# Kernel tuning notes

Measured on AMD Instinct MI355X. Metric: run time of the kernel, lower is better.

The kernel has to match this reference:

```python
import jax, jax.numpy as jnp
import numpy as np

EMBED_DIM = 1024
NUM_HEADS = 16
HEAD_DIM = EMBED_DIM // NUM_HEADS


def setup_inputs() -> dict:
    key = jax.random.key(0)
    k1, k2, k3, k4 = jax.random.split(key, 4)
    B, T, C = 4, 2048, EMBED_DIM
    scale = 1.0 / np.sqrt(C)
    x = jax.random.normal(k1, (B, T, C), dtype=jnp.float32)
    # nn.Linear(C, 3C, bias=False): weight [3C, C]
    w_qkv = jax.random.normal(k2, (3 * C, C), dtype=jnp.float32) * scale
    # nn.Linear(C, C) with bias
    w_out = jax.random.normal(k3, (C, C), dtype=jnp.float32) * scale
    b_out = jax.random.normal(k4, (C,), dtype=jnp.float32) * 0.01
    return {"x": x, "w_qkv": w_qkv, "w_out": w_out, "b_out": b_out}


def reference(x, w_qkv, w_out, b_out):
    B, T, C = x.shape
    H, D = NUM_HEADS, HEAD_DIM
    qkv = x @ w_qkv.T                      # [B,T,3C]
    q, k, v = jnp.split(qkv, 3, axis=-1)
    # [B,T,C] -> [B,H,T,D]
    q = q.reshape(B, T, H, D).transpose(0, 2, 1, 3)
    k = k.reshape(B, T, H, D).transpose(0, 2, 1, 3)
    v = v.reshape(B, T, H, D).transpose(0, 2, 1, 3)
    scores = jnp.einsum("bhqd,bhkd->bhqk", q, k) / jnp.sqrt(jnp.float32(D))
    causal = jnp.tril(jnp.ones((T, T), dtype=bool))
    scores = jnp.where(causal, scores, -jnp.inf)
    attn = jax.nn.softmax(scores, axis=-1)  # dropout is identity in eval mode
    out = jnp.einsum("bhqk,bhkd->bhqd", attn, v)
    out = out.transpose(0, 2, 1, 3).reshape(B, T, C)
    return out @ w_out.T + b_out
```

## Files before the change

kernel.cpp:

```cpp
#include <hip/hip_runtime.h>
#include <hip/hip_bf16.h>

typedef __bf16 bf16_t;
typedef __bf16 bf16x4 __attribute__((ext_vector_type(4)));
typedef __bf16 bf16x8 __attribute__((ext_vector_type(8)));
typedef float f32x4 __attribute__((ext_vector_type(4)));

#define MFMA16(a, b, c) __builtin_amdgcn_mfma_f32_16x16x32_bf16(a, b, c, 0, 0, 0)

__device__ __forceinline__ void gld16(const bf16_t* g, bf16_t* l) {
  __builtin_amdgcn_global_load_lds(
      (const __attribute__((address_space(1))) unsigned int*)(const void*)g,
      (__attribute__((address_space(3))) unsigned int*)(void*)l, 16, 0, 0);
}

__global__ __launch_bounds__(256) void cvt_f32_bf16(
    const float* __restrict__ src, bf16_t* __restrict__ dst, long long n) {
  long long i = ((long long)blockIdx.x * 256 + threadIdx.x) * 8;
  const long long stride = (long long)gridDim.x * 256 * 8;
  for (; i < n; i += stride) {
    f32x4 a = *(const f32x4*)(src + i);
    f32x4 b = *(const f32x4*)(src + i + 4);
    bf16x8 r;
#pragma unroll
    for (int e = 0; e < 4; ++e) {
      r[e] = (bf16_t)a[e];
      r[4 + e] = (bf16_t)b[e];
    }
    *(bf16x8*)(dst + i) = r;
  }
}

template <bool WF32, typename TC, bool BIAS>
__global__ __launch_bounds__(256, 2) void gemm_async(
    const bf16_t* __restrict__ A, int lda, const void* __restrict__ Wv,
    const float* __restrict__ bias, TC* __restrict__ C, int ldc,
    int M, int N, int K) {
  constexpr int BST = WF32 ? 40 : 32;
  __shared__ bf16_t As[128 * 32];
  __shared__ bf16_t Bs[128 * BST];

  const int tid = threadIdx.x;
  const int i = tid & 63;
  const int w = tid >> 6;
  const int l16 = tid & 15;
  const int quad = (tid >> 4) & 3;
  const int wm = w & 1;
  const int wn = w >> 1;
  const int m0 = blockIdx.y * 128;
  const int n0 = blockIdx.x * 128;

  const bf16_t* ag = A + (size_t)(m0 + w * 32 + (i >> 2)) * lda + (i & 3) * 8;
  bf16_t* as0 = &As[(w * 32) * 32];
  bf16_t* as1 = &As[(w * 32 + 16) * 32];

  const bf16_t* bg = nullptr;
  bf16_t *bs0 = nullptr, *bs1 = nullptr;
  const float* wfg = nullptr;
  bf16_t* bsw = nullptr;
  if (!WF32) {
    bg = (const bf16_t*)Wv + (size_t)(n0 + w * 32 + (i >> 2)) * K + (i & 3) * 8;
    bs0 = &Bs[(w * 32) * 32];
    bs1 = &Bs[(w * 32 + 16) * 32];
  } else {
    const int srow = tid >> 1;
    const int scol = (tid & 1) * 16;
    wfg = (const float*)Wv + (size_t)(n0 + srow) * K + scol;
    bsw = &Bs[srow * BST + scol];
  }

  f32x4 acc[4][4] = {};

  for (int k0 = 0; k0 < K; k0 += 32) {
    __syncthreads();
    gld16(ag + k0, as0);
    gld16(ag + 16 * lda + k0, as1);
    if (!WF32) {
      gld16(bg + k0, bs0);
      gld16(bg + 16 * K + k0, bs1);
    } else {
      f32x4 a = *(const f32x4*)(wfg + k0);
      f32x4 b = *(const f32x4*)(wfg + k0 + 4);
      f32x4 c2 = *(const f32x4*)(wfg + k0 + 8);
      f32x4 d = *(const f32x4*)(wfg + k0 + 12);
      bf16x8 r0, r1;
#pragma unroll
      for (int e = 0; e < 4; ++e) {
        r0[e] = (bf16_t)a[e];
        r0[4 + e] = (bf16_t)b[e];
        r1[e] = (bf16_t)c2[e];
        r1[4 + e] = (bf16_t)d[e];
      }
      *(bf16x8*)(bsw) = r0;
      *(bf16x8*)(bsw + 8) = r1;
    }
    __syncthreads();

    bf16x8 af[4], bfr[4];
#pragma unroll
    for (int t = 0; t < 4; ++t) {
      af[t] = *(const bf16x8*)&As[(wm * 64 + t * 16 + l16) * 32 + quad * 8];
      bfr[t] = *(const bf16x8*)&Bs[(wn * 64 + t * 16 + l16) * BST + quad * 8];
    }
#pragma unroll
    for (int mi = 0; mi < 4; ++mi)
#pragma unroll
      for (int ni = 0; ni < 4; ++ni)
        acc[mi][ni] = MFMA16(af[mi], bfr[ni], acc[mi][ni]);
  }

#pragma unroll
  for (int ni = 0; ni < 4; ++ni) {
    const int col = n0 + wn * 64 + ni * 16 + l16;
    const float bv = BIAS ? bias[col] : 0.0f;
#pragma unroll
    for (int mi = 0; mi < 4; ++mi) {
      const int row = m0 + wm * 64 + mi * 16 + quad * 4;
#pragma unroll
      for (int r = 0; r < 4; ++r)
        C[(size_t)(row + r) * ldc + col] = (TC)(acc[mi][ni][r] + bv);
    }
  }
}

__global__ __launch_bounds__(512, 4) void attn_mfma(bf16_t* __restrict__ qkv) {
  constexpr int T = 2048, C3 = 3072, C = 1024;
  __shared__ bf16_t Ks[64 * 72];
  __shared__ bf16_t Vt[64 * 72];
  __shared__ bf16_t Ps[8 * 16 * 72];

  const int tid = threadIdx.x;
  const int wave = tid >> 6;
  const int lane = tid & 63;
  const int l16 = tid & 15;
  const int quad = (tid >> 4) & 3;
  const int p = blockIdx.x;
  const int b = blockIdx.y >> 4;
  const int h = blockIdx.y & 15;
  bf16_t* base = qkv + (size_t)b * T * C3;

  const float QSCALE = 0.125f * 1.44269504088896340736f;

  const int kst = tid >> 2;
  const int ksd = (tid & 3) * 16;
  const int vtok = lane;
  const int vdg = (wave - 4) * 16;

  bf16_t* pw = &Ps[wave * 16 * 72];

  bf16x8 st0, st1;

  for (int s = 0; s < 2; ++s) {
    const int qt = (s == 0) ? p : 15 - p;
    const int Q0 = qt * 128;
    const int qlo = Q0 + wave * 16;
    const int jmax = Q0 + 64;

    bf16x8 qf[2];
    {
      const bf16_t* qp = base + (size_t)(qlo + l16) * C3 + h * 64 + quad * 8;
      bf16x8 a = *(const bf16x8*)qp;
      bf16x8 c = *(const bf16x8*)(qp + 32);
#pragma unroll
      for (int e = 0; e < 8; ++e) {
        a[e] = (bf16_t)((float)a[e] * QSCALE);
        c[e] = (bf16_t)((float)c[e] * QSCALE);
      }
      qf[0] = a;
      qf[1] = c;
    }

    f32x4 Of[4] = {};
    float mrow = -1e30f;
    float lrow = 0.f;

    if (wave < 4) {
      const bf16_t* kp = base + (size_t)kst * C3 + C + h * 64 + ksd;
      st0 = *(const bf16x8*)kp;
      st1 = *(const bf16x8*)(kp + 8);
    } else {
      const bf16_t* vp = base + (size_t)vtok * C3 + 2 * C + h * 64 + vdg;
      st0 = *(const bf16x8*)vp;
      st1 = *(const bf16x8*)(vp + 8);
    }

    for (int j0 = 0; j0 <= jmax; j0 += 64) {
      __syncthreads();
      if (wave < 4) {
        *(bf16x8*)&Ks[kst * 72 + ksd] = st0;
        *(bf16x8*)&Ks[kst * 72 + ksd + 8] = st1;
      } else {
#pragma unroll
        for (int e = 0; e < 8; ++e) {
          Vt[(vdg + e) * 72 + vtok] = st0[e];
          Vt[(vdg + 8 + e) * 72 + vtok] = st1[e];
        }
      }
      if (j0 + 64 <= jmax) {
        const int jn = j0 + 64;
        if (wave < 4) {
          const bf16_t* kp = base + (size_t)(jn + kst) * C3 + C + h * 64 + ksd;
          st0 = *(const bf16x8*)kp;
          st1 = *(const bf16x8*)(kp + 8);
        } else {
          const bf16_t* vp =
              base + (size_t)(jn + vtok) * C3 + 2 * C + h * 64 + vdg;
          st0 = *(const bf16x8*)vp;
          st1 = *(const bf16x8*)(vp + 8);
        }
      }
      __syncthreads();

      if (qlo + 15 < j0) continue;

      float Sv[4][4];
      const int qrow = qlo + l16;
      __builtin_amdgcn_s_setprio(1);
#pragma unroll
      for (int nt = 0; nt < 4; ++nt) {
        f32x4 sacc = {};
#pragma unroll
        for (int s2 = 0; s2 < 2; ++s2) {
          bf16x8 kf =
              *(const bf16x8*)&Ks[(nt * 16 + l16) * 72 + s2 * 32 + quad * 8];
          sacc = MFMA16(kf, qf[s2], sacc);
        }
#pragma unroll
        for (int r = 0; r < 4; ++r) Sv[nt][r] = sacc[r];
      }
      __builtin_amdgcn_s_setprio(0);

      if (j0 + 64 > qlo) {
#pragma unroll
        for (int nt = 0; nt < 4; ++nt) {
          const int keyb = j0 + nt * 16 + quad * 4;
#pragma unroll
          for (int r = 0; r < 4; ++r)
            if (keyb + r > qrow) Sv[nt][r] = -1e30f;
        }
      }

      float vm[4];
#pragma unroll
      for (int nt = 0; nt < 4; ++nt)
        vm[nt] = fmaxf(fmaxf(Sv[nt][0], Sv[nt][1]),
                       fmaxf(Sv[nt][2], Sv[nt][3]));
      float v = fmaxf(fmaxf(vm[0], vm[1]), fmaxf(vm[2], vm[3]));
      v = fmaxf(v, __shfl_xor(v, 16));
      v = fmaxf(v, __shfl_xor(v, 32));

      if (__any(v > mrow)) {
        const float mnew = fmaxf(mrow, v);
        const float alpha = __builtin_amdgcn_exp2f(mrow - mnew);
        mrow = mnew;
        lrow *= alpha;
        float ar[4];
#pragma unroll
        for (int r = 0; r < 4; ++r) ar[r] = __shfl(alpha, quad * 4 + r, 16);
#pragma unroll
        for (int dt = 0; dt < 4; ++dt)
#pragma unroll
          for (int r = 0; r < 4; ++r) Of[dt][r] *= ar[r];
      }

      float rsn[4];
#pragma unroll
      for (int nt = 0; nt < 4; ++nt) {
        bf16x4 pk;
        float r0 = __builtin_amdgcn_exp2f(Sv[nt][0] - mrow);
        float r1 = __builtin_amdgcn_exp2f(Sv[nt][1] - mrow);
        float r2 = __builtin_amdgcn_exp2f(Sv[nt][2] - mrow);
        float r3 = __builtin_amdgcn_exp2f(Sv[nt][3] - mrow);
        pk[0] = (bf16_t)r0;
        pk[1] = (bf16_t)r1;
        pk[2] = (bf16_t)r2;
        pk[3] = (bf16_t)r3;
        rsn[nt] = (r0 + r1) + (r2 + r3);
        *(bf16x4*)&pw[l16 * 72 + nt * 16 + quad * 4] = pk;
      }
      float rs = (rsn[0] + rsn[1]) + (rsn[2] + rsn[3]);
      rs += __shfl_xor(rs, 16);
      rs += __shfl_xor(rs, 32);
      lrow += rs;

      bf16x8 pf0 = *(const bf16x8*)&pw[l16 * 72 + quad * 8];
      bf16x8 pf1 = *(const bf16x8*)&pw[l16 * 72 + 32 + quad * 8];
      __builtin_amdgcn_s_setprio(1);
#pragma unroll
      for (int dt = 0; dt < 4; ++dt) {
        bf16x8 vf0 = *(const bf16x8*)&Vt[(dt * 16 + l16) * 72 + quad * 8];
        bf16x8 vf1 = *(const bf16x8*)&Vt[(dt * 16 + l16) * 72 + 32 + quad * 8];
        Of[dt] = MFMA16(pf0, vf0, Of[dt]);
        Of[dt] = MFMA16(pf1, vf1, Of[dt]);
      }
      __builtin_amdgcn_s_setprio(0);
    }

    float lr[4];
#pragma unroll
    for (int r = 0; r < 4; ++r) lr[r] = __shfl(lrow, quad * 4 + r, 16);
    const int t = Q0 + wave * 16 + quad * 4;
#pragma unroll
    for (int r = 0; r < 4; ++r) {
      const float inv = 1.0f / lr[r];
      bf16_t* op = base + (size_t)(t + r) * C3 + h * 64 + l16;
#pragma unroll
      for (int dt = 0; dt < 4; ++dt)
        op[dt * 16] = (bf16_t)(Of[dt][r] * inv);
    }
  }
}

extern "C" void kernel_launch(void* const* d_in, const int* in_sizes, int n_in,
                              void* d_out, int out_size, void* d_ws,
                              size_t ws_size, hipStream_t stream) {
  constexpr int B = 4, T = 2048, C = 1024;
  constexpr int M = B * T;

  const float* x = (const float*)d_in[0];
  const float* w_qkv = (const float*)d_in[1];
  const float* w_out = (const float*)d_in[2];
  const float* b_out = (const float*)d_in[3];
  for (int i = 0; i < n_in; ++i) {
    const long long s = in_sizes[i];
    if (s == (long long)M * C) x = (const float*)d_in[i];
    else if (s == (long long)3 * C * C) w_qkv = (const float*)d_in[i];
    else if (s == (long long)C * C) w_out = (const float*)d_in[i];
    else if (s == C) b_out = (const float*)d_in[i];
  }

  bf16_t* xb = (bf16_t*)d_out;
  bf16_t* wqb = xb + (size_t)M * C;
  bf16_t* qkv = (bf16_t*)d_ws;
  bf16_t* wob = qkv + (size_t)M * 3 * C;
  const bool ws_ok =
      ws_size >= (size_t)M * 3 * C * 2 + (size_t)C * C * 2;

  cvt_f32_bf16<<<1024, 256, 0, stream>>>(x, xb, (long long)M * C);
  cvt_f32_bf16<<<512, 256, 0, stream>>>(w_qkv, wqb, 3LL * C * C);
  if (ws_ok)
    cvt_f32_bf16<<<256, 256, 0, stream>>>(w_out, wob, (long long)C * C);

  gemm_async<false, bf16_t, false>
      <<<dim3(3 * C / 128, M / 128), 256, 0, stream>>>(
          xb, C, wqb, nullptr, qkv, 3 * C, M, 3 * C, C);

  attn_mfma<<<dim3(8, B * 16), 512, 0, stream>>>(qkv);

  if (ws_ok)
    gemm_async<false, float, true><<<dim3(C / 128, M / 128), 256, 0, stream>>>(
        qkv, 3 * C, wob, b_out, (float*)d_out, C, M, C, C);
  else
    gemm_async<true, float, true><<<dim3(C / 128, M / 128), 256, 0, stream>>>(
        qkv, 3 * C, w_out, b_out, (float*)d_out, C, M, C, C);
}
```

Baseline: 265.1 us.

## Double-buffer GEMM LDS tiles, prefetch next K slice, and swizzle workgroup order

Converts the GEMM main loop to a two-stage LDS pipeline: the next K tile is fetched with async global-to-LDS loads, or held in registers for the f32 weight path, while MFMAs run on the current tile. This removes one barrier per iteration and hides load latency. It also remaps workgroup IDs in groups of eight, likely to spread neighbouring tiles across XCDs, and raises wave priority around the MFMA block. The cost is doubled LDS, which may cut occupancy, and extra registers for the prefetched f32 values.

```diff
diff --git a/kernel.cpp b/kernel.cpp
--- a/kernel.cpp
+++ b/kernel.cpp
@@ -37,8 +37,8 @@
     const float* __restrict__ bias, TC* __restrict__ C, int ldc,
     int M, int N, int K) {
   constexpr int BST = WF32 ? 40 : 32;
-  __shared__ bf16_t As[128 * 32];
-  __shared__ bf16_t Bs[128 * BST];
+  __shared__ bf16_t As[2][128 * 32];
+  __shared__ bf16_t Bs[2][128 * BST];
 
   const int tid = threadIdx.x;
   const int i = tid & 63;
@@ -47,66 +47,110 @@
   const int quad = (tid >> 4) & 3;
   const int wm = w & 1;
   const int wn = w >> 1;
-  const int m0 = blockIdx.y * 128;
-  const int n0 = blockIdx.x * 128;
+
+  const int nwg = gridDim.x * gridDim.y;
+  int wg = blockIdx.y * gridDim.x + blockIdx.x;
+  if ((nwg & 7) == 0) wg = (wg & 7) * (nwg >> 3) + (wg >> 3);
+  const int m0 = (wg / gridDim.x) * 128;
+  const int n0 = (wg % gridDim.x) * 128;
 
   const bf16_t* ag = A + (size_t)(m0 + w * 32 + (i >> 2)) * lda + (i & 3) * 8;
-  bf16_t* as0 = &As[(w * 32) * 32];
-  bf16_t* as1 = &As[(w * 32 + 16) * 32];
+  bf16_t* as0[2] = {&As[0][(w * 32) * 32], &As[1][(w * 32) * 32]};
+  bf16_t* as1[2] = {&As[0][(w * 32 + 16) * 32], &As[1][(w * 32 + 16) * 32]};
 
   const bf16_t* bg = nullptr;
-  bf16_t *bs0 = nullptr, *bs1 = nullptr;
+  bf16_t *bs0[2] = {nullptr, nullptr}, *bs1[2] = {nullptr, nullptr};
   const float* wfg = nullptr;
-  bf16_t* bsw = nullptr;
+  bf16_t* bsw[2] = {nullptr, nullptr};
   if (!WF32) {
     bg = (const bf16_t*)Wv + (size_t)(n0 + w * 32 + (i >> 2)) * K + (i & 3) * 8;
-    bs0 = &Bs[(w * 32) * 32];
-    bs1 = &Bs[(w * 32 + 16) * 32];
+    bs0[0] = &Bs[0][(w * 32) * 32];
+    bs0[1] = &Bs[1][(w * 32) * 32];
+    bs1[0] = &Bs[0][(w * 32 + 16) * 32];
+    bs1[1] = &Bs[1][(w * 32 + 16) * 32];
   } else {
     const int srow = tid >> 1;
     const int scol = (tid & 1) * 16;
     wfg = (const float*)Wv + (size_t)(n0 + srow) * K + scol;
-    bsw = &Bs[srow * BST + scol];
+    bsw[0] = &Bs[0][srow * BST + scol];
+    bsw[1] = &Bs[1][srow * BST + scol];
   }
 
   f32x4 acc[4][4] = {};
 
+  gld16(ag, as0[0]);
+  gld16(ag + 16 * lda, as1[0]);
+  if (!WF32) {
+    gld16(bg, bs0[0]);
+    gld16(bg + 16 * K, bs1[0]);
+  } else {
+    f32x4 a = *(const f32x4*)(wfg);
+    f32x4 b = *(const f32x4*)(wfg + 4);
+    f32x4 c2 = *(const f32x4*)(wfg + 8);
+    f32x4 d = *(const f32x4*)(wfg + 12);
+    bf16x8 r0, r1;
+#pragma unroll
+    for (int e = 0; e < 4; ++e) {
+      r0[e] = (bf16_t)a[e];
+      r0[4 + e] = (bf16_t)b[e];
+      r1[e] = (bf16_t)c2[e];
+      r1[4 + e] = (bf16_t)d[e];
+    }
+    *(bf16x8*)(bsw[0]) = r0;
+    *(bf16x8*)(bsw[0] + 8) = r1;
+  }
+  __syncthreads();
+
+  int cur = 0;
   for (int k0 = 0; k0 < K; k0 += 32) {
-    __syncthreads();
-    gld16(ag + k0, as0);
-    gld16(ag + 16 * lda + k0, as1);
-    if (!WF32) {
-      gld16(bg + k0, bs0);
-      gld16(bg + 16 * K + k0, bs1);
-    } else {
-      f32x4 a = *(const f32x4*)(wfg + k0);
-      f32x4 b = *(const f32x4*)(wfg + k0 + 4);
-      f32x4 c2 = *(const f32x4*)(wfg + k0 + 8);
-      f32x4 d = *(const f32x4*)(wfg + k0 + 12);
-      bf16x8 r0, r1;
-#pragma unroll
-      for (int e = 0; e < 4; ++e) {
-        r0[e] = (bf16_t)a[e];
-        r0[4 + e] = (bf16_t)b[e];
-        r1[e] = (bf16_t)c2[e];
-        r1[4 + e] = (bf16_t)d[e];
-      }
-      *(bf16x8*)(bsw) = r0;
-      *(bf16x8*)(bsw + 8) = r1;
-    }
-    __syncthreads();
+    const bool has_next = (k0 + 32 < K);
+    const int nxt = cur ^ 1;
+    f32x4 wa, wb, wc, wd;
+
+    if (has_next) {
+      gld16(ag + k0 + 32, as0[nxt]);
+      gld16(ag + 16 * lda + k0 + 32, as1[nxt]);
+      if (!WF32) {
+        gld16(bg + k0 + 32, bs0[nxt]);
+        gld16(bg + 16 * K + k0 + 32, bs1[nxt]);
+      } else {
+        wa = *(const f32x4*)(wfg + k0 + 32);
+        wb = *(const f32x4*)(wfg + k0 + 36);
+        wc = *(const f32x4*)(wfg + k0 + 40);
+        wd = *(const f32x4*)(wfg + k0 + 44);
+      }
+    }
 
     bf16x8 af[4], bfr[4];
 #pragma unroll
     for (int t = 0; t < 4; ++t) {
-      af[t] = *(const bf16x8*)&As[(wm * 64 + t * 16 + l16) * 32 + quad * 8];
-      bfr[t] = *(const bf16x8*)&Bs[(wn * 64 + t * 16 + l16) * BST + quad * 8];
-    }
+      af[t] = *(const bf16x8*)&As[cur][(wm * 64 + t * 16 + l16) * 32 + quad * 8];
+      bfr[t] =
+          *(const bf16x8*)&Bs[cur][(wn * 64 + t * 16 + l16) * BST + quad * 8];
+    }
+    __builtin_amdgcn_s_setprio(1);
 #pragma unroll
     for (int mi = 0; mi < 4; ++mi)
 #pragma unroll
       for (int ni = 0; ni < 4; ++ni)
         acc[mi][ni] = MFMA16(af[mi], bfr[ni], acc[mi][ni]);
+    __builtin_amdgcn_s_setprio(0);
+
+    if (WF32 && has_next) {
+      bf16x8 r0, r1;
+#pragma unroll
+      for (int e = 0; e < 4; ++e) {
+        r0[e] = (bf16_t)wa[e];
+        r0[4 + e] = (bf16_t)wb[e];
+        r1[e] = (bf16_t)wc[e];
+        r1[4 + e] = (bf16_t)wd[e];
+      }
+      *(bf16x8*)(bsw[nxt]) = r0;
+      *(bf16x8*)(bsw[nxt] + 8) = r1;
+    }
+
+    __syncthreads();
+    cur = nxt;
   }
 
 #pragma unroll
```

New measurement: 260.5 us. Within noise of the previous version (-1.7%).
